# Kernel optimization log

Measured on AMD Instinct MI355X. Metric: run time of the kernel, lower is better.

## Reference

```python
import jax, jax.numpy as jnp
import numpy as np

M, IN, OUT, K = 16384, 1024, 1024, 12


def setup_inputs() -> dict:
    key = jax.random.key(0)
    ks = jax.random.split(key, 7)
    x = jax.random.normal(ks[0], (M, IN), dtype=jnp.float32)
    # grid: per-feature linspace(-2,2) plus noise so the per-row sort is nontrivial
    base = jnp.linspace(-2.0, 2.0, K, dtype=jnp.float32)
    grid = jnp.broadcast_to(base, (IN, K)) + 0.3 * jax.random.normal(ks[1], (IN, K), dtype=jnp.float32)
    coeffs = 0.1 * jax.random.normal(ks[2], (IN, K), dtype=jnp.float32)
    knot_alive = 3.0 * jnp.ones((IN, K), dtype=jnp.float32) + 0.5 * jax.random.normal(ks[3], (IN, K), dtype=jnp.float32)
    proj_w = jax.random.normal(ks[4], (OUT, IN), dtype=jnp.float32) / np.sqrt(IN)
    proj_b = jax.random.normal(ks[5], (OUT,), dtype=jnp.float32) * 0.01
    res_w = jax.random.normal(ks[6], (OUT, IN), dtype=jnp.float32) / np.sqrt(IN)
    return {"x": x, "grid": grid, "coeffs": coeffs, "knot_alive": knot_alive,
            "proj_w": proj_w, "proj_b": proj_b, "res_w": res_w}


def _eval_adaptive_spline(x, grid, coeffs, knot_alive):
    # x: (M, in)  grid/coeffs/knot_alive: (in, K)
    K_ = grid.shape[1]
    sort_idx = jnp.argsort(grid, axis=1)
    sorted_grid = jnp.take_along_axis(grid, sort_idx, axis=1)
    sorted_coeffs = jnp.take_along_axis(coeffs, sort_idx, axis=1)
    sorted_alive = jnp.take_along_axis(knot_alive, sort_idx, axis=1)
    masked_coeffs = sorted_coeffs * jax.nn.sigmoid(sorted_alive)  # (in, K)

    grid_min = sorted_grid[:, 0]   # (in,)
    grid_max = sorted_grid[:, -1]  # (in,)
    x_clamped = jnp.minimum(jnp.maximum(x, grid_min[None, :]), grid_max[None, :])
    grid_range = jnp.maximum(grid_max - grid_min, 1e-6)
    x_norm = (x_clamped - grid_min[None, :]) / grid_range[None, :] * (K_ - 1)  # (M, in)
    idx_l = jnp.clip(x_norm.astype(jnp.int32), 0, K_ - 2)  # trunc == floor (x_norm >= 0)
    frac = x_norm - idx_l.astype(x.dtype)

    feat = jnp.arange(x.shape[1])[None, :]  # (1, in)
    c_left = masked_coeffs[feat, idx_l]      # (M, in)
    c_right = masked_coeffs[feat, idx_l + 1]  # (M, in)
    return c_left + frac * (c_right - c_left)


def reference(x, grid, coeffs, knot_alive, proj_w, proj_b, res_w):
    spline_out = _eval_adaptive_spline(x, grid, coeffs, knot_alive)  # (M, in)
    return spline_out @ proj_w.T + proj_b + x @ res_w.T  # (M, out)
```

## Files before the change

### kernel.cpp

```cpp
#include <hip/hip_runtime.h>
#include <hip/hip_bf16.h>

typedef unsigned short u16;
typedef float f32x4 __attribute__((ext_vector_type(4)));
typedef __bf16 bf16x8 __attribute__((ext_vector_type(8)));
typedef u16 u16x8 __attribute__((ext_vector_type(8)));

#define M_DIM 16384
#define IN_DIM 1024
#define OUT_DIM 1024
#define K_KNOTS 12
#define KCAT 2048


__device__ __forceinline__ u16 f2bf(float f) {
    unsigned int u = __builtin_bit_cast(unsigned int, f);
    u = u + 0x7FFFu + ((u >> 16) & 1u);
    return (u16)(u >> 16);
}

__device__ __forceinline__ void gload_lds16(const void* g, void* l) {
    __builtin_amdgcn_global_load_lds(
        (const __attribute__((address_space(1))) unsigned int*)g,
        (__attribute__((address_space(3))) unsigned int*)l, 16, 0, 0);
}

__global__ void prep_kernel(const float* __restrict__ grid,
                            const float* __restrict__ coeffs,
                            const float* __restrict__ alive,
                            float* __restrict__ pmc,
                            float* __restrict__ pgmin,
                            float* __restrict__ pscale)
{
    int i = blockIdx.x * blockDim.x + threadIdx.x;
    if (i >= IN_DIM) return;
    float g[K_KNOTS], c[K_KNOTS], a[K_KNOTS];
    for (int k = 0; k < K_KNOTS; ++k) {
        g[k] = grid[i * K_KNOTS + k];
        c[k] = coeffs[i * K_KNOTS + k];
        a[k] = alive[i * K_KNOTS + k];
    }
    for (int k = 1; k < K_KNOTS; ++k) {
        float gk = g[k], ck = c[k], ak = a[k];
        int j = k - 1;
        while (j >= 0 && g[j] > gk) {
            g[j + 1] = g[j]; c[j + 1] = c[j]; a[j + 1] = a[j]; --j;
        }
        g[j + 1] = gk; c[j + 1] = ck; a[j + 1] = ak;
    }
    for (int k = 0; k < K_KNOTS; ++k)
        pmc[i * K_KNOTS + k] = c[k] / (1.0f + expf(-a[k]));
    pgmin[i] = g[0];
    pscale[i] = (float)(K_KNOTS - 1) / fmaxf(g[K_KNOTS - 1] - g[0], 1e-6f);
}

__global__ __launch_bounds__(256) void conv_w_kernel(
    const float* __restrict__ pw, const float* __restrict__ rw,
    u16* __restrict__ Bw)
{
    const int n16 = blockIdx.x;
    const int tid = threadIdx.x;
    #pragma unroll 1
    for (int j = 0; j < 16; ++j) {
        int s = j * 256 + tid;
        int kc = s >> 6, l = s & 63;
        int row = n16 * 16 + (l & 15);
        int k = kc * 32 + ((l >> 4) & 3) * 8;
        const float* src = (k < IN_DIM) ? &pw[(long)row * IN_DIM + k]
                                        : &rw[(long)row * IN_DIM + (k - IN_DIM)];
        float4 v0 = *(const float4*)src;
        float4 v1 = *(const float4*)(src + 4);
        u16x8 ov;
        ov[0] = f2bf(v0.x); ov[1] = f2bf(v0.y); ov[2] = f2bf(v0.z); ov[3] = f2bf(v0.w);
        ov[4] = f2bf(v1.x); ov[5] = f2bf(v1.y); ov[6] = f2bf(v1.z); ov[7] = f2bf(v1.w);
        *(u16x8*)&Bw[((long)n16 * 64 + kc) * 512 + l * 8] = ov;
    }
}

#define XT_STR 260

__global__ __launch_bounds__(512) void build_a_kernel(
    const float* __restrict__ x,
    const float* __restrict__ pmc,
    const float* __restrict__ pgmin,
    const float* __restrict__ pscale,
    u16* __restrict__ Abf)
{
    __shared__ float s_mc[IN_DIM * K_KNOTS];
    __shared__ float s_gmin[IN_DIM];
    __shared__ float s_scale[IN_DIM];
    __shared__ float xt[16 * XT_STR];
    const int tid = threadIdx.x;
    for (int i = tid; i < IN_DIM * K_KNOTS; i += 512) s_mc[i] = pmc[i];
    for (int i = tid; i < IN_DIM; i += 512) { s_gmin[i] = pgmin[i]; s_scale[i] = pscale[i]; }

    #pragma unroll 1
    for (int g = 0; g < 4; ++g) {
        const int m16 = blockIdx.x * 4 + g;
        #pragma unroll 1
        for (int c0 = 0; c0 < IN_DIM; c0 += 256) {
            __syncthreads();

            #pragma unroll
            for (int p = 0; p < 2; ++p) {
                int idx = p * 512 + tid;
                int r = idx >> 6, lc = (idx & 63) * 4;
                float4 v = *(const float4*)&x[(long)(m16 * 16 + r) * IN_DIM + c0 + lc];
                *(float4*)&xt[r * XT_STR + lc] = v;
            }
            __syncthreads();

            {
                int kc_l = tid >> 6, l = tid & 63;
                int r = l & 15;
                int cb = kc_l * 32 + ((l >> 4) & 3) * 8;
                const float* xp = &xt[r * XT_STR + cb];
                float4 v0 = *(const float4*)xp;
                float4 v1 = *(const float4*)(xp + 4);
                float xs[8] = {v0.x, v0.y, v0.z, v0.w, v1.x, v1.y, v1.z, v1.w};
                u16x8 so, co;
                #pragma unroll
                for (int e = 0; e < 8; ++e) {
                    int i = c0 + cb + e;
                    float xx = xs[e];
                    float xn = (xx - s_gmin[i]) * s_scale[i];
                    xn = fminf(fmaxf(xn, 0.0f), (float)(K_KNOTS - 1));
                    int li = (int)xn;
                    if (li > K_KNOTS - 2) li = K_KNOTS - 2;
                    float frac = xn - (float)li;
                    float cl = s_mc[i * K_KNOTS + li];
                    float cr = s_mc[i * K_KNOTS + li + 1];
                    so[e] = f2bf(cl + frac * (cr - cl));
                    co[e] = f2bf(xx);
                }
                long kcS = (long)m16 * 64 + (c0 >> 5) + kc_l;
                *(u16x8*)&Abf[kcS * 512 + l * 8] = so;
                *(u16x8*)&Abf[(kcS + 32) * 512 + l * 8] = co;
            }
        }
    }
}

#define TBK 32
#define NT (KCAT / TBK)
#define MSTR 32768L

#define BAR()     asm volatile("s_barrier" ::: "memory")
#define VM3BAR()  asm volatile("s_waitcnt vmcnt(3)\ns_barrier" ::: "memory")
#define LGKM0()   do { asm volatile("s_waitcnt lgkmcnt(0)" ::: "memory"); \
                       __builtin_amdgcn_sched_barrier(0); } while (0)

#define STAGE2(T, cb) do { \
    gload_lds16(pAf +          ((long)(T)) * 512, &lds[(cb) * 4096 + tid * 8]); \
    gload_lds16(pBf +          ((long)(T)) * 512, &lds[8192 + (cb) * 8192 + tid * 8]); \
    gload_lds16(pBf + 8*MSTR + ((long)(T)) * 512, &lds[8192 + (cb) * 8192 + 4096 + tid * 8]); } while (0)

__global__ __launch_bounds__(512, 4) void gemm_kernel(
    const u16* __restrict__ A,
    const u16* __restrict__ B,
    const float* __restrict__ bias,
    float* __restrict__ C)
{
    __shared__ __align__(16) u16 lds[24576];

    const int tid  = threadIdx.x;
    const int lane = tid & 63;
    const int wave = tid >> 6;
    const int wm   = wave >> 2;
    const int wn   = wave & 3;

    int wgid = (blockIdx.x & 7) * 64 + (blockIdx.x >> 3);
    const int brow = (wgid >> 2) * 128;
    const int bcol = (wgid & 3) * 256;

    const u16* pAf = A + ((long)(brow >> 4) + wave) * MSTR + lane * 8;
    const u16* pBf = B + ((long)(bcol >> 4) + wave) * MSTR + lane * 8;

    const int loff = lane * 8;

    f32x4 acc[4][4] = {};
    bf16x8 af[4], bfr[4];

    STAGE2(0, 0);
    STAGE2(1, 1);
    VM3BAR();

    #pragma unroll 1
    for (int t = 0; t < NT; ++t) {
        const int cb = t & 1;
        const int ab = cb * 4096;
        const int bb = 8192 + cb * 8192;

        #pragma unroll
        for (int m_ = 0; m_ < 4; ++m_)
            af[m_] = *(const bf16x8*)&lds[ab + (wm * 4 + m_) * 512 + loff];
        #pragma unroll
        for (int n_ = 0; n_ < 4; ++n_)
            bfr[n_] = *(const bf16x8*)&lds[bb + (wn * 4 + n_) * 512 + loff];
        LGKM0();
        __builtin_amdgcn_s_setprio(1);
        #pragma unroll
        for (int m_ = 0; m_ < 4; ++m_)
            #pragma unroll
            for (int n_ = 0; n_ < 4; ++n_)
                acc[m_][n_] = __builtin_amdgcn_mfma_f32_16x16x32_bf16(
                    af[m_], bfr[n_], acc[m_][n_], 0, 0, 0);
        __builtin_amdgcn_s_setprio(0);
        BAR();

        const int T2 = (t + 2) & 63;
        STAGE2(T2, cb);
        VM3BAR();
    }

    const int crow0 = brow + wm * 64 + (lane >> 4) * 4;
    const int ccol0 = bcol + wn * 64 + (lane & 15);
    float bv[4];
    #pragma unroll
    for (int n = 0; n < 4; ++n) bv[n] = bias[ccol0 + n * 16];
    #pragma unroll
    for (int m = 0; m < 4; ++m) {
        #pragma unroll
        for (int n = 0; n < 4; ++n) {
            #pragma unroll
            for (int j = 0; j < 4; ++j) {
                int row = crow0 + m * 16 + j;
                C[(long)row * OUT_DIM + ccol0 + n * 16] = acc[m][n][j] + bv[n];
            }
        }
    }
}

extern "C" void kernel_launch(void* const* d_in, const int* in_sizes, int n_in,
                              void* d_out, int out_size, void* d_ws, size_t ws_size,
                              hipStream_t stream) {
    const float* x      = (const float*)d_in[0];
    const float* grid   = (const float*)d_in[1];
    const float* coeffs = (const float*)d_in[2];
    const float* alive  = (const float*)d_in[3];
    const float* proj_w = (const float*)d_in[4];
    const float* proj_b = (const float*)d_in[5];
    const float* res_w  = (const float*)d_in[6];
    float* out = (float*)d_out;

    char* w = (char*)d_ws;
    size_t a_bytes = (size_t)M_DIM * KCAT * sizeof(u16);
    size_t b_bytes = (size_t)OUT_DIM * KCAT * sizeof(u16);
    u16* Abf   = (u16*)w;
    u16* Bw    = (u16*)(w + a_bytes);
    float* pmc = (float*)(w + a_bytes + b_bytes);
    float* pgmin  = pmc + IN_DIM * K_KNOTS;
    float* pscale = pgmin + IN_DIM;

    prep_kernel<<<(IN_DIM + 255) / 256, 256, 0, stream>>>(grid, coeffs, alive,
                                                          pmc, pgmin, pscale);
    conv_w_kernel<<<OUT_DIM / 16, 256, 0, stream>>>(proj_w, res_w, Bw);
    build_a_kernel<<<M_DIM / 64, 512, 0, stream>>>(x, pmc, pgmin, pscale, Abf);
    gemm_kernel<<<(M_DIM / 128) * (OUT_DIM / 256), 512, 0, stream>>>(Abf, Bw, proj_b, out);
}
```

Before: 108.4 us.

## Shrink GEMM tile to 128x128 with 4 waves and split weight conversion blocks

After: 111.3 us. +2.6%, slower.

```diff
diff --git a/kernel.cpp b/kernel.cpp
--- a/kernel.cpp
+++ b/kernel.cpp
@@ -58,10 +58,11 @@
     const float* __restrict__ pw, const float* __restrict__ rw,
     u16* __restrict__ Bw)
 {
-    const int n16 = blockIdx.x;
+    const int n16 = blockIdx.x >> 2;
+    const int jb  = (blockIdx.x & 3) * 4;
     const int tid = threadIdx.x;
     #pragma unroll 1
-    for (int j = 0; j < 16; ++j) {
+    for (int j = jb; j < jb + 4; ++j) {
         int s = j * 256 + tid;
         int kc = s >> 6, l = s & 63;
         int row = n16 * 16 + (l & 15);
@@ -146,32 +147,34 @@
 #define MSTR 32768L
 
 #define BAR()     asm volatile("s_barrier" ::: "memory")
-#define VM3BAR()  asm volatile("s_waitcnt vmcnt(3)\ns_barrier" ::: "memory")
+#define VM4BAR()  asm volatile("s_waitcnt vmcnt(4)\ns_barrier" ::: "memory")
 #define LGKM0()   do { asm volatile("s_waitcnt lgkmcnt(0)" ::: "memory"); \
                        __builtin_amdgcn_sched_barrier(0); } while (0)
 
-#define STAGE2(T, cb) do { \
-    gload_lds16(pAf +          ((long)(T)) * 512, &lds[(cb) * 4096 + tid * 8]); \
-    gload_lds16(pBf +          ((long)(T)) * 512, &lds[8192 + (cb) * 8192 + tid * 8]); \
-    gload_lds16(pBf + 8*MSTR + ((long)(T)) * 512, &lds[8192 + (cb) * 8192 + 4096 + tid * 8]); } while (0)
-
-__global__ __launch_bounds__(512, 4) void gemm_kernel(
+#define STAGE4(T, cb) do { \
+    gload_lds16(pAf +          ((long)(T)) * 512, &lds[(cb) * 4096 + wave * 512 + lane * 8]); \
+    gload_lds16(pAf + 4*MSTR + ((long)(T)) * 512, &lds[(cb) * 4096 + (wave + 4) * 512 + lane * 8]); \
+    gload_lds16(pBf +          ((long)(T)) * 512, &lds[8192 + (cb) * 4096 + wave * 512 + lane * 8]); \
+    gload_lds16(pBf + 4*MSTR + ((long)(T)) * 512, &lds[8192 + (cb) * 4096 + (wave + 4) * 512 + lane * 8]); } while (0)
+
+__global__ __launch_bounds__(256, 4) void gemm_kernel(
     const u16* __restrict__ A,
     const u16* __restrict__ B,
     const float* __restrict__ bias,
     float* __restrict__ C)
 {
-    __shared__ __align__(16) u16 lds[24576];
+    __shared__ __align__(16) u16 lds[16384];
 
     const int tid  = threadIdx.x;
     const int lane = tid & 63;
     const int wave = tid >> 6;
-    const int wm   = wave >> 2;
-    const int wn   = wave & 3;
-
-    int wgid = (blockIdx.x & 7) * 64 + (blockIdx.x >> 3);
-    const int brow = (wgid >> 2) * 128;
-    const int bcol = (wgid & 3) * 256;
+    const int wm   = wave >> 1;
+    const int wn   = wave & 1;
+
+    const int rp = blockIdx.x & 127;
+    const int cc = blockIdx.x >> 7;
+    const int brow = rp * 128;
+    const int bcol = cc * 128;
 
     const u16* pAf = A + ((long)(brow >> 4) + wave) * MSTR + lane * 8;
     const u16* pBf = B + ((long)(bcol >> 4) + wave) * MSTR + lane * 8;
@@ -181,15 +184,15 @@
     f32x4 acc[4][4] = {};
     bf16x8 af[4], bfr[4];
 
-    STAGE2(0, 0);
-    STAGE2(1, 1);
-    VM3BAR();
+    STAGE4(0, 0);
+    STAGE4(1, 1);
+    VM4BAR();
 
     #pragma unroll 1
     for (int t = 0; t < NT; ++t) {
         const int cb = t & 1;
         const int ab = cb * 4096;
-        const int bb = 8192 + cb * 8192;
+        const int bb = 8192 + cb * 4096;
 
         #pragma unroll
         for (int m_ = 0; m_ < 4; ++m_)
@@ -209,8 +212,8 @@
         BAR();
 
         const int T2 = (t + 2) & 63;
-        STAGE2(T2, cb);
-        VM3BAR();
+        STAGE4(T2, cb);
+        VM4BAR();
     }
 
     const int crow0 = brow + wm * 64 + (lane >> 4) * 4;
@@ -254,7 +257,7 @@
 
     prep_kernel<<<(IN_DIM + 255) / 256, 256, 0, stream>>>(grid, coeffs, alive,
                                                           pmc, pgmin, pscale);
-    conv_w_kernel<<<OUT_DIM / 16, 256, 0, stream>>>(proj_w, res_w, Bw);
+    conv_w_kernel<<<(OUT_DIM / 16) * 4, 256, 0, stream>>>(proj_w, res_w, Bw);
     build_a_kernel<<<M_DIM / 64, 512, 0, stream>>>(x, pmc, pgmin, pscale, Abf);
-    gemm_kernel<<<(M_DIM / 128) * (OUT_DIM / 256), 512, 0, stream>>>(Abf, Bw, proj_b, out);
-}
+    gemm_kernel<<<(M_DIM / 128) * (OUT_DIM / 128), 256, 0, stream>>>(Abf, Bw, proj_b, out);
+}
```

## Switch GEMM to 32x32x16 MFMA with matching 32-row fragment layouts

Applied to the files above, without the earlier changes.

After: 114.2 us. 1.05x slower.

```diff
diff --git a/kernel.cpp b/kernel.cpp
--- a/kernel.cpp
+++ b/kernel.cpp
@@ -2,7 +2,7 @@
 #include <hip/hip_bf16.h>
 
 typedef unsigned short u16;
-typedef float f32x4 __attribute__((ext_vector_type(4)));
+typedef float f32x16 __attribute__((ext_vector_type(16)));
 typedef __bf16 bf16x8 __attribute__((ext_vector_type(8)));
 typedef u16 u16x8 __attribute__((ext_vector_type(8)));
 
@@ -12,6 +12,7 @@
 #define K_KNOTS 12
 #define KCAT 2048
 
+#define GSTR 65536L
 
 __device__ __forceinline__ u16 f2bf(float f) {
     unsigned int u = __builtin_bit_cast(unsigned int, f);
@@ -58,14 +59,15 @@
     const float* __restrict__ pw, const float* __restrict__ rw,
     u16* __restrict__ Bw)
 {
-    const int n16 = blockIdx.x;
+    const int n32 = blockIdx.x >> 3;
+    const int kb  = (blockIdx.x & 7) * 256;
     const int tid = threadIdx.x;
     #pragma unroll 1
-    for (int j = 0; j < 16; ++j) {
-        int s = j * 256 + tid;
-        int kc = s >> 6, l = s & 63;
-        int row = n16 * 16 + (l & 15);
-        int k = kc * 32 + ((l >> 4) & 3) * 8;
+    for (int it = 0; it < 4; ++it) {
+        int q = it * 256 + tid;
+        int k16l = q >> 6, l = q & 63;
+        int row = n32 * 32 + (l & 31);
+        int k = kb + k16l * 16 + (l >> 5) * 8;
         const float* src = (k < IN_DIM) ? &pw[(long)row * IN_DIM + k]
                                         : &rw[(long)row * IN_DIM + (k - IN_DIM)];
         float4 v0 = *(const float4*)src;
@@ -73,11 +75,11 @@
         u16x8 ov;
         ov[0] = f2bf(v0.x); ov[1] = f2bf(v0.y); ov[2] = f2bf(v0.z); ov[3] = f2bf(v0.w);
         ov[4] = f2bf(v1.x); ov[5] = f2bf(v1.y); ov[6] = f2bf(v1.z); ov[7] = f2bf(v1.w);
-        *(u16x8*)&Bw[((long)n16 * 64 + kc) * 512 + l * 8] = ov;
-    }
-}
-
-#define XT_STR 260
+        *(u16x8*)&Bw[((long)n32 * 128 + (kb >> 4) + k16l) * 512 + l * 8] = ov;
+    }
+}
+
+#define XT2 132
 
 __global__ __launch_bounds__(512) void build_a_kernel(
     const float* __restrict__ x,
@@ -89,53 +91,53 @@
     __shared__ float s_mc[IN_DIM * K_KNOTS];
     __shared__ float s_gmin[IN_DIM];
     __shared__ float s_scale[IN_DIM];
-    __shared__ float xt[16 * XT_STR];
+    __shared__ float xt[32 * XT2];
     const int tid = threadIdx.x;
     for (int i = tid; i < IN_DIM * K_KNOTS; i += 512) s_mc[i] = pmc[i];
     for (int i = tid; i < IN_DIM; i += 512) { s_gmin[i] = pgmin[i]; s_scale[i] = pscale[i]; }
 
     #pragma unroll 1
-    for (int g = 0; g < 4; ++g) {
-        const int m16 = blockIdx.x * 4 + g;
+    for (int gg = 0; gg < 2; ++gg) {
+        const int g32 = blockIdx.x * 2 + gg;
         #pragma unroll 1
-        for (int c0 = 0; c0 < IN_DIM; c0 += 256) {
+        for (int c0 = 0; c0 < IN_DIM; c0 += 128) {
             __syncthreads();
 
             #pragma unroll
             for (int p = 0; p < 2; ++p) {
-                int idx = p * 512 + tid;
-                int r = idx >> 6, lc = (idx & 63) * 4;
-                float4 v = *(const float4*)&x[(long)(m16 * 16 + r) * IN_DIM + c0 + lc];
-                *(float4*)&xt[r * XT_STR + lc] = v;
+                int q = p * 512 + tid;
+                int r = q >> 5, cl = (q & 31) * 4;
+                float4 v = *(const float4*)&x[(long)(g32 * 32 + r) * IN_DIM + c0 + cl];
+                *(float4*)&xt[r * XT2 + cl] = v;
             }
             __syncthreads();
 
             {
-                int kc_l = tid >> 6, l = tid & 63;
-                int r = l & 15;
-                int cb = kc_l * 32 + ((l >> 4) & 3) * 8;
-                const float* xp = &xt[r * XT_STR + cb];
+                int k16l = tid >> 6, l = tid & 63;
+                int row = l & 31;
+                int colc = k16l * 16 + (l >> 5) * 8;
+                const float* xp = &xt[row * XT2 + colc];
                 float4 v0 = *(const float4*)xp;
                 float4 v1 = *(const float4*)(xp + 4);
                 float xs[8] = {v0.x, v0.y, v0.z, v0.w, v1.x, v1.y, v1.z, v1.w};
                 u16x8 so, co;
                 #pragma unroll
                 for (int e = 0; e < 8; ++e) {
-                    int i = c0 + cb + e;
+                    int i = c0 + colc + e;
                     float xx = xs[e];
                     float xn = (xx - s_gmin[i]) * s_scale[i];
                     xn = fminf(fmaxf(xn, 0.0f), (float)(K_KNOTS - 1));
                     int li = (int)xn;
                     if (li > K_KNOTS - 2) li = K_KNOTS - 2;
                     float frac = xn - (float)li;
-                    float cl = s_mc[i * K_KNOTS + li];
-                    float cr = s_mc[i * K_KNOTS + li + 1];
-                    so[e] = f2bf(cl + frac * (cr - cl));
+                    float cl_ = s_mc[i * K_KNOTS + li];
+                    float cr_ = s_mc[i * K_KNOTS + li + 1];
+                    so[e] = f2bf(cl_ + frac * (cr_ - cl_));
                     co[e] = f2bf(xx);
                 }
-                long kcS = (long)m16 * 64 + (c0 >> 5) + kc_l;
-                *(u16x8*)&Abf[kcS * 512 + l * 8] = so;
-                *(u16x8*)&Abf[(kcS + 32) * 512 + l * 8] = co;
+                long gk16 = (c0 >> 4) + k16l;
+                *(u16x8*)&Abf[((long)g32 * 128 + gk16) * 512 + l * 8] = so;
+                *(u16x8*)&Abf[((long)g32 * 128 + gk16 + 64) * 512 + l * 8] = co;
             }
         }
     }
@@ -143,17 +145,16 @@
 
 #define TBK 32
 #define NT (KCAT / TBK)
-#define MSTR 32768L
-
+
+#define VM3BAR()  asm volatile("s_waitcnt vmcnt(3)\ns_barrier" ::: "memory")
 #define BAR()     asm volatile("s_barrier" ::: "memory")
-#define VM3BAR()  asm volatile("s_waitcnt vmcnt(3)\ns_barrier" ::: "memory")
 #define LGKM0()   do { asm volatile("s_waitcnt lgkmcnt(0)" ::: "memory"); \
                        __builtin_amdgcn_sched_barrier(0); } while (0)
 
-#define STAGE2(T, cb) do { \
-    gload_lds16(pAf +          ((long)(T)) * 512, &lds[(cb) * 4096 + tid * 8]); \
-    gload_lds16(pBf +          ((long)(T)) * 512, &lds[8192 + (cb) * 8192 + tid * 8]); \
-    gload_lds16(pBf + 8*MSTR + ((long)(T)) * 512, &lds[8192 + (cb) * 8192 + 4096 + tid * 8]); } while (0)
+#define STAGE3(T, cb) do { \
+    gload_lds16(pAg + (long)(T) * 1024,       &lds[(cb) * 4096 + tid * 8]); \
+    gload_lds16(pBg + (long)(T) * 1024,       &lds[8192 + (cb) * 8192 + tid * 8]); \
+    gload_lds16(pBg + (long)(T) * 1024 + 512, &lds[8192 + (cb) * 8192 + 4096 + tid * 8]); } while (0)
 
 __global__ __launch_bounds__(512, 4) void gemm_kernel(
     const u16* __restrict__ A,
@@ -173,16 +174,17 @@
     const int brow = (wgid >> 2) * 128;
     const int bcol = (wgid & 3) * 256;
 
-    const u16* pAf = A + ((long)(brow >> 4) + wave) * MSTR + lane * 8;
-    const u16* pBf = B + ((long)(bcol >> 4) + wave) * MSTR + lane * 8;
+    const u16* pAg = A + ((long)(brow >> 5) + ((tid >> 6) & 3)) * GSTR
+                       + (long)(tid >> 8) * 512 + lane * 8;
+    const u16* pBg = B + ((long)(bcol >> 5) + (tid >> 6)) * GSTR + lane * 8;
 
     const int loff = lane * 8;
 
-    f32x4 acc[4][4] = {};
-    bf16x8 af[4], bfr[4];
-
-    STAGE2(0, 0);
-    STAGE2(1, 1);
+    f32x16 acc[2][2] = {};
+    bf16x8 af[2][2], bf[2][2];
+
+    STAGE3(0, 0);
+    STAGE3(1, 1);
     VM3BAR();
 
     #pragma unroll 1
@@ -192,40 +194,45 @@
         const int bb = 8192 + cb * 8192;
 
         #pragma unroll
-        for (int m_ = 0; m_ < 4; ++m_)
-            af[m_] = *(const bf16x8*)&lds[ab + (wm * 4 + m_) * 512 + loff];
-        #pragma unroll
-        for (int n_ = 0; n_ < 4; ++n_)
-            bfr[n_] = *(const bf16x8*)&lds[bb + (wn * 4 + n_) * 512 + loff];
+        for (int kl = 0; kl < 2; ++kl) {
+            #pragma unroll
+            for (int mi = 0; mi < 2; ++mi)
+                af[kl][mi] = *(const bf16x8*)&lds[ab + (kl * 4 + wm * 2 + mi) * 512 + loff];
+            #pragma unroll
+            for (int ni = 0; ni < 2; ++ni)
+                bf[kl][ni] = *(const bf16x8*)&lds[bb + (kl * 8 + wn * 2 + ni) * 512 + loff];
+        }
         LGKM0();
         __builtin_amdgcn_s_setprio(1);
         #pragma unroll
-        for (int m_ = 0; m_ < 4; ++m_)
-            #pragma unroll
-            for (int n_ = 0; n_ < 4; ++n_)
-                acc[m_][n_] = __builtin_amdgcn_mfma_f32_16x16x32_bf16(
-                    af[m_], bfr[n_], acc[m_][n_], 0, 0, 0);
+        for (int kl = 0; kl < 2; ++kl)
+            #pragma unroll
+            for (int mi = 0; mi < 2; ++mi)
+                #pragma unroll
+                for (int ni = 0; ni < 2; ++ni)
+                    acc[mi][ni] = __builtin_amdgcn_mfma_f32_32x32x16_bf16(
+                        af[kl][mi], bf[kl][ni], acc[mi][ni], 0, 0, 0);
         __builtin_amdgcn_s_setprio(0);
         BAR();
 
         const int T2 = (t + 2) & 63;
-        STAGE2(T2, cb);
+        STAGE3(T2, cb);
         VM3BAR();
     }
 
-    const int crow0 = brow + wm * 64 + (lane >> 4) * 4;
-    const int ccol0 = bcol + wn * 64 + (lane & 15);
-    float bv[4];
+    const int row0 = brow + wm * 64 + 4 * (lane >> 5);
+    const int col0 = bcol + wn * 64 + (lane & 31);
+    float bv[2];
     #pragma unroll
-    for (int n = 0; n < 4; ++n) bv[n] = bias[ccol0 + n * 16];
+    for (int ni = 0; ni < 2; ++ni) bv[ni] = bias[col0 + ni * 32];
     #pragma unroll
-    for (int m = 0; m < 4; ++m) {
+    for (int mi = 0; mi < 2; ++mi) {
         #pragma unroll
-        for (int n = 0; n < 4; ++n) {
-            #pragma unroll
-            for (int j = 0; j < 4; ++j) {
-                int row = crow0 + m * 16 + j;
-                C[(long)row * OUT_DIM + ccol0 + n * 16] = acc[m][n][j] + bv[n];
+        for (int ni = 0; ni < 2; ++ni) {
+            #pragma unroll
+            for (int reg = 0; reg < 16; ++reg) {
+                int row = row0 + mi * 32 + (reg & 3) + 8 * (reg >> 2);
+                C[(long)row * OUT_DIM + col0 + ni * 32] = acc[mi][ni][reg] + bv[ni];
             }
         }
     }
@@ -254,7 +261,7 @@
 
     prep_kernel<<<(IN_DIM + 255) / 256, 256, 0, stream>>>(grid, coeffs, alive,
                                                           pmc, pgmin, pscale);
-    conv_w_kernel<<<OUT_DIM / 16, 256, 0, stream>>>(proj_w, res_w, Bw);
+    conv_w_kernel<<<256, 256, 0, stream>>>(proj_w, res_w, Bw);
     build_a_kernel<<<M_DIM / 64, 512, 0, stream>>>(x, pmc, pgmin, pscale, Abf);
     gemm_kernel<<<(M_DIM / 128) * (OUT_DIM / 256), 512, 0, stream>>>(Abf, Bw, proj_b, out);
 }
```
